# Performance work log

Measured on AMD Instinct MI355X. Metric: run time of the kernel, lower is better.

The kernel has to match this reference:

```python
import jax, jax.numpy as jnp
import numpy as np

N = 100000
E = 1600000
DIN = 128
HID = 64
DOUT = 40
LAYERS = 8
ALPHA = 0.1
THETA = 0.5


def setup_inputs() -> dict:
    key = jax.random.key(0)
    ks = jax.random.split(key, 8)
    x = jax.random.normal(ks[0], (N, DIN), dtype=jnp.float32)
    edge_index = jax.random.randint(ks[1], (2, E), 0, N, dtype=jnp.int64)
    s1 = 1.0 / np.sqrt(DIN)
    s2 = 1.0 / np.sqrt(HID)
    W1 = jax.random.uniform(ks[2], (DIN, HID), jnp.float32, -s1, s1)
    b1 = jax.random.uniform(ks[3], (HID,), jnp.float32, -s1, s1)
    conv_ws = jax.random.uniform(ks[4], (LAYERS, HID, HID), jnp.float32, -s2, s2)
    W2 = jax.random.uniform(ks[5], (HID, DOUT), jnp.float32, -s2, s2)
    b2 = jax.random.uniform(ks[6], (DOUT,), jnp.float32, -s2, s2)
    return {"x": x, "edge_index": edge_index, "W1": W1, "b1": b1,
            "conv_ws": conv_ws, "W2": W2, "b2": b2}


def reference(x, edge_index, W1, b1, conv_ws, W2, b2):
    n = x.shape[0]
    # gcn_norm with self-loops: Ahat = D^-1/2 (A + I) D^-1/2
    loop = jnp.arange(n, dtype=edge_index.dtype)
    src = jnp.concatenate([edge_index[0], loop])
    dst = jnp.concatenate([edge_index[1], loop])
    deg = jax.ops.segment_sum(jnp.ones_like(src, dtype=x.dtype), dst, num_segments=n)
    dinv = jnp.where(deg > 0, jax.lax.rsqrt(deg), 0.0)
    w_e = dinv[src] * dinv[dst]  # [E+N]

    h0 = h = jax.nn.relu(x @ W1 + b1)  # [N, HID]
    for i in range(LAYERS):
        agg = jax.ops.segment_sum(h[src] * w_e[:, None], dst, num_segments=n)
        out = (1.0 - ALPHA) * agg + ALPHA * h0
        beta = np.log(THETA / (i + 1) + 1.0).astype(np.float32)
        h = jax.nn.relu((1.0 - beta) * out + beta * (out @ conv_ws[i]))
    return h @ W2 + b2
```

## Files before the change

kernel.cpp:

```cpp
#include <hip/hip_runtime.h>
#include <hip/hip_fp16.h>
#include <stdint.h>
#include <math.h>

#define HID 64
#define DIN 128
#define DOUT 40
#define N_LAYERS 8
#define CSR_CAP 768

typedef _Float16 half8 __attribute__((ext_vector_type(8)));
typedef float f32x4 __attribute__((ext_vector_type(4)));

static inline int cdiv(int a, int b) { return (a + b - 1) / b; }

__device__ __forceinline__ int edge_src(const uint32_t* ei, int is64, int E, int e) {
    return is64 ? (int)ei[2 * e] : (int)ei[e];
}
__device__ __forceinline__ int edge_dst(const uint32_t* ei, int is64, int E, int e) {
    return is64 ? (int)ei[2 * (size_t)E + 2 * e] : (int)ei[(size_t)E + e];
}

__global__ void setup(const uint32_t* __restrict__ ei, int* __restrict__ flag,
                      const float* __restrict__ convw, __half* __restrict__ Bp,
                      const float* __restrict__ W1, __half* __restrict__ W1h,
                      int* __restrict__ cnt, int n, int nb) {
    int b = blockIdx.x;
    int t = threadIdx.x;
    if (b < nb) {
        int v = b * 256 + t;
        if (v < n) cnt[v] = 0;
        return;
    }
    int r = b - nb;
    if (r < N_LAYERS) {
        float beta = logf(0.5f / (float)(r + 1) + 1.f);
        const float* W = convw + (size_t)r * HID * HID;
        __half* out = Bp + (size_t)r * HID * HID;
        for (int idx = t; idx < HID * HID; idx += 256) {
            int k = idx >> 6, nn = idx & 63;
            float v = beta * W[k * HID + nn] + ((k == nn) ? (1.f - beta) : 0.f);
            out[nn * HID + k] = __float2half(v);
        }
    } else if (r == N_LAYERS) {
        for (int idx = t; idx < DIN * HID; idx += 256) {
            int nn = idx >> 7, k = idx & 127;
            W1h[nn * DIN + k] = __float2half(W1[k * HID + nn]);
        }
    } else if (r == N_LAYERS + 1) {
        if (t < 64) {
            uint32_t wv = ei[2 * t + 1];
            unsigned long long nz = __ballot(wv != 0u);
            if (t == 0) *flag = (nz == 0ull) ? 1 : 0;
        }
    }
}

__global__ void count_pos(const uint32_t* __restrict__ ei, const int* __restrict__ flag,
                          int* __restrict__ cnt, int* __restrict__ pw,
                          int e0, int e1, int E) {
    int e = e0 + blockIdx.x * blockDim.x + threadIdx.x;
    if (e >= e1) return;
    int is64 = *flag;
    int d = edge_dst(ei, is64, E, e);
    pw[e] = atomicAdd(&cnt[d], 1);
}

__global__ void scan1(const int* __restrict__ cnt, int* __restrict__ row_start,
                      int* __restrict__ blocksum, int n) {
    __shared__ int sh[256];
    int t = threadIdx.x;
    int v = blockIdx.x * 256 + t;
    int val = (v < n) ? cnt[v] : 0;
    sh[t] = val;
    __syncthreads();
    for (int o = 1; o < 256; o <<= 1) {
        int y = (t >= o) ? sh[t - o] : 0;
        __syncthreads();
        sh[t] += y;
        __syncthreads();
    }
    if (v < n) row_start[v] = sh[t] - val;
    if (t == 255) blocksum[blockIdx.x] = sh[255];
}

__global__ void scan2(int* __restrict__ blocksum, int nb) {
    __shared__ int sh[512];
    int t = threadIdx.x;
    int val = (t < nb) ? blocksum[t] : 0;
    sh[t] = val;
    __syncthreads();
    for (int o = 1; o < 512; o <<= 1) {
        int y = (t >= o) ? sh[t - o] : 0;
        __syncthreads();
        sh[t] += y;
        __syncthreads();
    }
    if (t < nb) blocksum[t] = sh[t] - val;
}

__global__ void scan3(int* __restrict__ row_start, const int* __restrict__ blocksum,
                      const int* __restrict__ cnt, float* __restrict__ dinv, int n) {
    int v = blockIdx.x * 256 + threadIdx.x;
    if (v < n) {
        row_start[v] += blocksum[v >> 8];
        dinv[v] = rsqrtf((float)(cnt[v] + 1));
    }
}

__global__ void scatter_pos(const uint32_t* __restrict__ ei, const int* __restrict__ flag,
                            const int* __restrict__ row_start, const int* __restrict__ pw,
                            int* __restrict__ csr_src, int E) {
    int e = blockIdx.x * blockDim.x + threadIdx.x;
    if (e >= E) return;
    int is64 = *flag;
    int s = edge_src(ei, is64, E, e);
    int d = edge_dst(ei, is64, E, e);
    csr_src[row_start[d] + pw[e]] = s;
}

__global__ void __launch_bounds__(256) mlp_in_mfma(
        const float* __restrict__ x, const __half* __restrict__ W1h,
        const float* __restrict__ b1, const float* __restrict__ dinv,
        __half2* __restrict__ hp2, __half2* __restrict__ h0h2, int n) {
    __shared__ __align__(16) ushort Bs[64 * 136];
    __shared__ __align__(16) ushort As[128 * 136];
    int t = threadIdx.x;
    {
        const __half2* W2 = (const __half2*)W1h;
        for (int i = t; i < 64 * 64; i += 256) {
            int bn = i >> 6, kp = i & 63;
            *(__half2*)&Bs[bn * 136 + 2 * kp] = W2[bn * 64 + kp];
        }
    }
    int node0 = blockIdx.x * 128;
    {
        const float4* x4 = (const float4*)x;
        for (int i = t; i < 128 * 32; i += 256) {
            int nd = i >> 5, q = i & 31;
            int node = node0 + nd;
            float4 xv = (node < n) ? x4[(size_t)node * 32 + q]
                                   : make_float4(0.f, 0.f, 0.f, 0.f);
            *(__half2*)&As[nd * 136 + q * 4]     = __floats2half2_rn(xv.x, xv.y);
            *(__half2*)&As[nd * 136 + q * 4 + 2] = __floats2half2_rn(xv.z, xv.w);
        }
    }
    __syncthreads();
    int lane = t & 63, wv = t >> 6;
    int nl = lane & 15, quad = lane >> 4;
    int m_base = wv * 32;
    f32x4 C[2][4];
#pragma unroll
    for (int mt = 0; mt < 2; mt++)
#pragma unroll
        for (int nt = 0; nt < 4; nt++) C[mt][nt] = (f32x4)0.f;
#pragma unroll
    for (int kc = 0; kc < 4; kc++) {
        half8 a[2], b[4];
#pragma unroll
        for (int mt = 0; mt < 2; mt++)
            a[mt] = *(const half8*)&As[(m_base + mt * 16 + nl) * 136 + kc * 32 + quad * 8];
#pragma unroll
        for (int nt = 0; nt < 4; nt++)
            b[nt] = *(const half8*)&Bs[(nt * 16 + nl) * 136 + kc * 32 + quad * 8];
#pragma unroll
        for (int mt = 0; mt < 2; mt++)
#pragma unroll
            for (int nt = 0; nt < 4; nt++)
                C[mt][nt] = __builtin_amdgcn_mfma_f32_16x16x32_f16(a[mt], b[nt],
                                                                   C[mt][nt], 0, 0, 0);
    }
    __syncthreads();
#pragma unroll
    for (int nt = 0; nt < 4; nt++) {
        float bias = b1[nt * 16 + nl];
#pragma unroll
        for (int mt = 0; mt < 2; mt++) {
#pragma unroll
            for (int reg = 0; reg < 4; reg++) {
                int nd = m_base + mt * 16 + quad * 4 + reg;
                float v = fmaxf(C[mt][nt][reg] + bias, 0.f);
                As[nd * 72 + nt * 16 + nl] = __half_as_ushort(__float2half(v));
            }
        }
    }
    __syncthreads();
    for (int i = t; i < 128 * 32; i += 256) {
        int nd = i >> 5, kp = i & 31;
        int node = node0 + nd;
        if (node < n) {
            __half2 h = *(const __half2*)&As[nd * 72 + 2 * kp];
            h0h2[(size_t)node * 32 + kp] = h;
            float dv = dinv[node];
            float2 f = __half22float2(h);
            hp2[(size_t)node * 32 + kp] = __floats2half2_rn(f.x * dv, f.y * dv);
        }
    }
}

__global__ void __launch_bounds__(256) gcnii_fused(
        const __half* __restrict__ hp, const __half* __restrict__ h0,
        const int* __restrict__ row_start, const int* __restrict__ cnt,
        const int* __restrict__ csr_src, const float* __restrict__ dinv,
        const __half* __restrict__ Bp, int scale_out,
        __half* __restrict__ hpn, int n, int E) {
    __shared__ __align__(16) ushort Bs[64 * 72];
    __shared__ __align__(16) ushort As[32 * 72];
    __shared__ int csr_lds[CSR_CAP];
    __shared__ int rs_lds[33];
    int t = threadIdx.x;
    int node0 = blockIdx.x * 32;
    int grp = t >> 3, sub = t & 7;

    for (int i = t; i < 512; i += 256) {
        int bn = i >> 3, s8 = i & 7;
        *(half8*)&Bs[bn * 72 + s8 * 8] = *(const half8*)(Bp + bn * 64 + s8 * 8);
    }
    int ts = row_start[node0];
    int te = (node0 + 32 < n) ? row_start[node0 + 32] : E;
    int ne = te - ts;
    int staged = ne < CSR_CAP ? ne : CSR_CAP;
    for (int i = t; i < staged; i += 256) csr_lds[i] = csr_src[ts + i];
    if (t < 33) {
        int v = node0 + t;
        rs_lds[t] = ((v < n) ? row_start[v] : E) - ts;
    }
    __syncthreads();

    int v = node0 + grp;
    int j = rs_lds[grp];
    int end = rs_lds[grp + 1];
    float acc[8];
#pragma unroll
    for (int q = 0; q < 8; q++) acc[q] = 0.f;
    if (ne <= CSR_CAP) {
        int e = j;
        for (; e + 4 <= end; e += 4) {
            int s0 = csr_lds[e],     s1 = csr_lds[e + 1];
            int s2 = csr_lds[e + 2], s3 = csr_lds[e + 3];
            if ((unsigned)s0 >= (unsigned)n) s0 = 0;
            if ((unsigned)s1 >= (unsigned)n) s1 = 0;
            if ((unsigned)s2 >= (unsigned)n) s2 = 0;
            if ((unsigned)s3 >= (unsigned)n) s3 = 0;
            half8 h0v = *(const half8*)(hp + (size_t)s0 * 64 + sub * 8);
            half8 h1v = *(const half8*)(hp + (size_t)s1 * 64 + sub * 8);
            half8 h2v = *(const half8*)(hp + (size_t)s2 * 64 + sub * 8);
            half8 h3v = *(const half8*)(hp + (size_t)s3 * 64 + sub * 8);
#pragma unroll
            for (int q = 0; q < 8; q++)
                acc[q] += ((float)h0v[q] + (float)h1v[q]) + ((float)h2v[q] + (float)h3v[q]);
        }
        for (; e < end; ++e) {
            int s = csr_lds[e];
            if ((unsigned)s >= (unsigned)n) s = 0;
            half8 hv = *(const half8*)(hp + (size_t)s * 64 + sub * 8);
#pragma unroll
            for (int q = 0; q < 8; q++) acc[q] += (float)hv[q];
        }
    } else {
        for (int e = j; e < end; ++e) {
            int s = csr_src[ts + e];
            if ((unsigned)s >= (unsigned)n) s = 0;
            half8 hv = *(const half8*)(hp + (size_t)s * 64 + sub * 8);
#pragma unroll
            for (int q = 0; q < 8; q++) acc[q] += (float)hv[q];
        }
    }
    {
        half8 o;
        if (v < n) {
            float sc = 0.9f * dinv[v];
            half8 hsv = *(const half8*)(hp + (size_t)v * 64 + sub * 8);
            half8 h0v = *(const half8*)(h0 + (size_t)v * 64 + sub * 8);
#pragma unroll
            for (int q = 0; q < 8; q++)
                o[q] = (_Float16)(sc * (acc[q] + (float)hsv[q]) + 0.1f * (float)h0v[q]);
        } else {
#pragma unroll
            for (int q = 0; q < 8; q++) o[q] = (_Float16)0.f;
        }
        *(half8*)&As[grp * 72 + sub * 8] = o;
    }
    __syncthreads();
    int lane = t & 63, w = t >> 6;
    int nl = lane & 15, quad = lane >> 4;
    int strip = w & 1, nth = w >> 1;
    f32x4 C[2];
    C[0] = (f32x4)0.f; C[1] = (f32x4)0.f;
#pragma unroll
    for (int kc = 0; kc < 2; kc++) {
        half8 a = *(const half8*)&As[(strip * 16 + nl) * 72 + kc * 32 + quad * 8];
#pragma unroll
        for (int t2 = 0; t2 < 2; t2++) {
            int nt = nth * 2 + t2;
            half8 b = *(const half8*)&Bs[(nt * 16 + nl) * 72 + kc * 32 + quad * 8];
            C[t2] = __builtin_amdgcn_mfma_f32_16x16x32_f16(a, b, C[t2], 0, 0, 0);
        }
    }
    __syncthreads();
#pragma unroll
    for (int reg = 0; reg < 4; reg++) {
        int nd = strip * 16 + quad * 4 + reg;
        int node = node0 + nd;
        float dv = (scale_out && node < n) ? dinv[node] : 1.f;
#pragma unroll
        for (int t2 = 0; t2 < 2; t2++) {
            int nt = nth * 2 + t2;
            float vv = fmaxf(C[t2][reg], 0.f) * dv;
            As[nd * 72 + nt * 16 + nl] = __half_as_ushort(__float2half(vv));
        }
    }
    __syncthreads();
    {
        int nd = t >> 3, s8 = t & 7;
        int node = node0 + nd;
        if (node < n)
            *(half8*)(hpn + (size_t)node * 64 + s8 * 8) = *(const half8*)&As[nd * 72 + s8 * 8];
    }
}

__global__ void mlp_out(const __half* __restrict__ h, const float* __restrict__ W2,
                        const float* __restrict__ b2, float* __restrict__ y, int n) {
    __shared__ float hs[32 * HID];
    __shared__ float W2s[HID * DOUT];
    __shared__ float b2s[DOUT];
    int t = threadIdx.x;
    for (int i = t; i < HID * DOUT; i += 256) W2s[i] = W2[i];
    if (t < DOUT) b2s[t] = b2[t];
    int node0 = blockIdx.x * 32;
    for (int i = t; i < 32 * HID; i += 256) {
        int node = node0 + (i >> 6);
        hs[i] = (node < n) ? __half2float(h[(size_t)node0 * HID + i]) : 0.f;
    }
    __syncthreads();
    for (int idx = t; idx < 32 * DOUT; idx += 256) {
        int nloc = idx / DOUT, fo = idx % DOUT;
        int node = node0 + nloc;
        if (node >= n) continue;
        float dot = b2s[fo];
#pragma unroll 8
        for (int k = 0; k < HID; k++) dot += hs[nloc * HID + k] * W2s[k * DOUT + fo];
        y[(size_t)node * DOUT + fo] = dot;
    }
}

extern "C" void kernel_launch(void* const* d_in, const int* in_sizes, int n_in,
                              void* d_out, int out_size, void* d_ws, size_t ws_size,
                              hipStream_t stream) {
    const float*    x     = (const float*)d_in[0];
    const uint32_t* ei    = (const uint32_t*)d_in[1];
    const float*    W1    = (const float*)d_in[2];
    const float*    b1    = (const float*)d_in[3];
    const float*    convw = (const float*)d_in[4];
    const float*    W2    = (const float*)d_in[5];
    const float*    b2    = (const float*)d_in[6];
    float*          y     = (float*)d_out;

    int N = in_sizes[0] / DIN;
    int E = in_sizes[1] / 2;

    char* ws = (char*)d_ws;
    size_t off = 0;
    auto alloc = [&](size_t bytes) -> char* {
        char* p = ws + off;
        off = (off + bytes + 255) & ~(size_t)255;
        return p;
    };
    int*     flag      = (int*)alloc(4);
    int*     cnt       = (int*)alloc((size_t)N * 4);
    int*     row_start = (int*)alloc((size_t)N * 4);
    float*   dinv      = (float*)alloc((size_t)N * 4);
    int*     blocksum  = (int*)alloc(512 * 4);
    int*     pw        = (int*)alloc((size_t)E * 4);
    int*     csr_src   = (int*)alloc((size_t)E * 4);
    __half*  Bp        = (__half*)alloc((size_t)N_LAYERS * HID * HID * 2);
    __half*  W1h       = (__half*)alloc((size_t)DIN * HID * 2);
    __half*  h0h       = (__half*)alloc((size_t)N * HID * 2);
    __half*  hpA       = (__half*)alloc((size_t)N * HID * 2);
    __half*  hpB       = (__half*)alloc((size_t)N * HID * 2);

    int nb = cdiv(N, 256);
    setup<<<nb + N_LAYERS + 2, 256, 0, stream>>>(ei, flag, convw, Bp, W1, W1h, cnt, N, nb);
    int Eh = E / 2;
    count_pos<<<cdiv(Eh, 256), 256, 0, stream>>>(ei, flag, cnt, pw, 0, Eh, E);
    count_pos<<<cdiv(E - Eh, 256), 256, 0, stream>>>(ei, flag, cnt, pw, Eh, E, E);
    scan1<<<nb, 256, 0, stream>>>(cnt, row_start, blocksum, N);
    scan2<<<1, 512, 0, stream>>>(blocksum, nb);
    scan3<<<cdiv(N, 256), 256, 0, stream>>>(row_start, blocksum, cnt, dinv, N);
    scatter_pos<<<cdiv(E, 256), 256, 0, stream>>>(ei, flag, row_start, pw, csr_src, E);

    mlp_in_mfma<<<cdiv(N, 128), 256, 0, stream>>>(x, W1h, b1, dinv,
                                                  (__half2*)hpA, (__half2*)h0h, N);

    __half* cur = hpA;
    __half* nxt = hpB;
    for (int i = 0; i < N_LAYERS; i++) {
        int scale_out = (i < N_LAYERS - 1) ? 1 : 0;
        gcnii_fused<<<cdiv(N, 32), 256, 0, stream>>>(
            cur, h0h, row_start, cnt, csr_src, dinv,
            Bp + (size_t)i * HID * HID, scale_out, nxt, N, E);
        __half* tmp = cur; cur = nxt; nxt = tmp;
    }
    mlp_out<<<cdiv(N, 32), 256, 0, stream>>>(cur, W2, b2, y, N);
}
```

Baseline: 531.9 us.

## Fuse output projection into last GCNII layer and simplify CSR build

Removes the separate mlp_out kernel. The final GCNII layer now computes the output projection with MFMA, using W2 split into hi and lo fp16 parts to keep precision. The per-edge position array is replaced by atomic cursor increments in scatter_pos, which saves E ints of writes and reads. The conv weight matrix is no longer staged in LDS and is read directly from global memory per MFMA operand. The last layer also skips writing the hidden state. Risks: CSR order within each row becomes nondeterministic, and B loads from global memory may be slower than from LDS.

```diff
diff --git a/kernel.cpp b/kernel.cpp
--- a/kernel.cpp
+++ b/kernel.cpp
@@ -24,7 +24,8 @@
 __global__ void setup(const uint32_t* __restrict__ ei, int* __restrict__ flag,
                       const float* __restrict__ convw, __half* __restrict__ Bp,
                       const float* __restrict__ W1, __half* __restrict__ W1h,
-                      int* __restrict__ cnt, int n, int nb) {
+                      const float* __restrict__ W2, __half* __restrict__ W2h,
+                      __half* __restrict__ W2l, int* __restrict__ cnt, int n, int nb) {
     int b = blockIdx.x;
     int t = threadIdx.x;
     if (b < nb) {
@@ -53,17 +54,24 @@
             unsigned long long nz = __ballot(wv != 0u);
             if (t == 0) *flag = (nz == 0ull) ? 1 : 0;
         }
+    } else {
+        for (int idx = t; idx < 48 * 64; idx += 256) {
+            int nn = idx >> 6, k = idx & 63;
+            float v = (nn < DOUT) ? W2[k * DOUT + nn] : 0.f;
+            __half hi = __float2half(v);
+            W2h[idx] = hi;
+            W2l[idx] = __float2half(v - __half2float(hi));
+        }
     }
 }
 
 __global__ void count_pos(const uint32_t* __restrict__ ei, const int* __restrict__ flag,
-                          int* __restrict__ cnt, int* __restrict__ pw,
-                          int e0, int e1, int E) {
+                          int* __restrict__ cnt, int e0, int e1, int E) {
     int e = e0 + blockIdx.x * blockDim.x + threadIdx.x;
     if (e >= e1) return;
     int is64 = *flag;
     int d = edge_dst(ei, is64, E, e);
-    pw[e] = atomicAdd(&cnt[d], 1);
+    atomicAdd(&cnt[d], 1);
 }
 
 __global__ void scan1(const int* __restrict__ cnt, int* __restrict__ row_start,
@@ -100,23 +108,25 @@
 }
 
 __global__ void scan3(int* __restrict__ row_start, const int* __restrict__ blocksum,
-                      const int* __restrict__ cnt, float* __restrict__ dinv, int n) {
+                      const int* __restrict__ cnt, int* __restrict__ ptr,
+                      float* __restrict__ dinv, int n) {
     int v = blockIdx.x * 256 + threadIdx.x;
     if (v < n) {
-        row_start[v] += blocksum[v >> 8];
+        int rs = row_start[v] + blocksum[v >> 8];
+        row_start[v] = rs;
+        ptr[v] = rs;
         dinv[v] = rsqrtf((float)(cnt[v] + 1));
     }
 }
 
 __global__ void scatter_pos(const uint32_t* __restrict__ ei, const int* __restrict__ flag,
-                            const int* __restrict__ row_start, const int* __restrict__ pw,
-                            int* __restrict__ csr_src, int E) {
+                            int* __restrict__ ptr, int* __restrict__ csr_src, int E) {
     int e = blockIdx.x * blockDim.x + threadIdx.x;
     if (e >= E) return;
     int is64 = *flag;
     int s = edge_src(ei, is64, E, e);
     int d = edge_dst(ei, is64, E, e);
-    csr_src[row_start[d] + pw[e]] = s;
+    csr_src[atomicAdd(&ptr[d], 1)] = s;
 }
 
 __global__ void __launch_bounds__(256) mlp_in_mfma(
@@ -127,10 +137,10 @@
     __shared__ __align__(16) ushort As[128 * 136];
     int t = threadIdx.x;
     {
-        const __half2* W2 = (const __half2*)W1h;
+        const __half2* W2v = (const __half2*)W1h;
         for (int i = t; i < 64 * 64; i += 256) {
             int bn = i >> 6, kp = i & 63;
-            *(__half2*)&Bs[bn * 136 + 2 * kp] = W2[bn * 64 + kp];
+            *(__half2*)&Bs[bn * 136 + 2 * kp] = W2v[bn * 64 + kp];
         }
     }
     int node0 = blockIdx.x * 128;
@@ -200,11 +210,11 @@
 
 __global__ void __launch_bounds__(256) gcnii_fused(
         const __half* __restrict__ hp, const __half* __restrict__ h0,
-        const int* __restrict__ row_start, const int* __restrict__ cnt,
-        const int* __restrict__ csr_src, const float* __restrict__ dinv,
-        const __half* __restrict__ Bp, int scale_out,
-        __half* __restrict__ hpn, int n, int E) {
-    __shared__ __align__(16) ushort Bs[64 * 72];
+        const int* __restrict__ row_start, const int* __restrict__ csr_src,
+        const float* __restrict__ dinv, const __half* __restrict__ Bp,
+        const __half* __restrict__ W2h, const __half* __restrict__ W2l,
+        const float* __restrict__ b2, int is_last,
+        __half* __restrict__ hpn, float* __restrict__ y, int n, int E) {
     __shared__ __align__(16) ushort As[32 * 72];
     __shared__ int csr_lds[CSR_CAP];
     __shared__ int rs_lds[33];
@@ -212,10 +222,6 @@
     int node0 = blockIdx.x * 32;
     int grp = t >> 3, sub = t & 7;
 
-    for (int i = t; i < 512; i += 256) {
-        int bn = i >> 3, s8 = i & 7;
-        *(half8*)&Bs[bn * 72 + s8 * 8] = *(const half8*)(Bp + bn * 64 + s8 * 8);
-    }
     int ts = row_start[node0];
     int te = (node0 + 32 < n) ? row_start[node0 + 32] : E;
     int ne = te - ts;
@@ -293,54 +299,52 @@
 #pragma unroll
         for (int t2 = 0; t2 < 2; t2++) {
             int nt = nth * 2 + t2;
-            half8 b = *(const half8*)&Bs[(nt * 16 + nl) * 72 + kc * 32 + quad * 8];
+            half8 b = *(const half8*)(Bp + (nt * 16 + nl) * 64 + kc * 32 + quad * 8);
             C[t2] = __builtin_amdgcn_mfma_f32_16x16x32_f16(a, b, C[t2], 0, 0, 0);
         }
     }
     __syncthreads();
-#pragma unroll
-    for (int reg = 0; reg < 4; reg++) {
-        int nd = strip * 16 + quad * 4 + reg;
-        int node = node0 + nd;
-        float dv = (scale_out && node < n) ? dinv[node] : 1.f;
-#pragma unroll
-        for (int t2 = 0; t2 < 2; t2++) {
-            int nt = nth * 2 + t2;
-            float vv = fmaxf(C[t2][reg], 0.f) * dv;
-            As[nd * 72 + nt * 16 + nl] = __half_as_ushort(__float2half(vv));
-        }
-    }
-    __syncthreads();
     {
+#pragma unroll
+        for (int reg = 0; reg < 4; reg++) {
+            int nd = strip * 16 + quad * 4 + reg;
+            int node = node0 + nd;
+            float dv = (!is_last && node < n) ? dinv[node] : 1.f;
+#pragma unroll
+            for (int t2 = 0; t2 < 2; t2++) {
+                int nt = nth * 2 + t2;
+                float vv = fmaxf(C[t2][reg], 0.f) * dv;
+                As[nd * 72 + nt * 16 + nl] = __half_as_ushort(__float2half(vv));
+            }
+        }
+    }
+    __syncthreads();
+    if (!is_last) {
         int nd = t >> 3, s8 = t & 7;
         int node = node0 + nd;
         if (node < n)
             *(half8*)(hpn + (size_t)node * 64 + s8 * 8) = *(const half8*)&As[nd * 72 + s8 * 8];
-    }
-}
-
-__global__ void mlp_out(const __half* __restrict__ h, const float* __restrict__ W2,
-                        const float* __restrict__ b2, float* __restrict__ y, int n) {
-    __shared__ float hs[32 * HID];
-    __shared__ float W2s[HID * DOUT];
-    __shared__ float b2s[DOUT];
-    int t = threadIdx.x;
-    for (int i = t; i < HID * DOUT; i += 256) W2s[i] = W2[i];
-    if (t < DOUT) b2s[t] = b2[t];
-    int node0 = blockIdx.x * 32;
-    for (int i = t; i < 32 * HID; i += 256) {
-        int node = node0 + (i >> 6);
-        hs[i] = (node < n) ? __half2float(h[(size_t)node0 * HID + i]) : 0.f;
-    }
-    __syncthreads();
-    for (int idx = t; idx < 32 * DOUT; idx += 256) {
-        int nloc = idx / DOUT, fo = idx % DOUT;
-        int node = node0 + nloc;
-        if (node >= n) continue;
-        float dot = b2s[fo];
-#pragma unroll 8
-        for (int k = 0; k < HID; k++) dot += hs[nloc * HID + k] * W2s[k * DOUT + fo];
-        y[(size_t)node * DOUT + fo] = dot;
+    } else {
+        for (int ct = (w >> 1); ct < 3; ct += 2) {
+            f32x4 C2 = (f32x4)0.f;
+#pragma unroll
+            for (int kc = 0; kc < 2; kc++) {
+                half8 a  = *(const half8*)&As[(strip * 16 + nl) * 72 + kc * 32 + quad * 8];
+                half8 bh = *(const half8*)(W2h + (ct * 16 + nl) * 64 + kc * 32 + quad * 8);
+                half8 bl = *(const half8*)(W2l + (ct * 16 + nl) * 64 + kc * 32 + quad * 8);
+                C2 = __builtin_amdgcn_mfma_f32_16x16x32_f16(a, bh, C2, 0, 0, 0);
+                C2 = __builtin_amdgcn_mfma_f32_16x16x32_f16(a, bl, C2, 0, 0, 0);
+            }
+            int col = ct * 16 + nl;
+            float bias = (col < DOUT) ? b2[col] : 0.f;
+#pragma unroll
+            for (int reg = 0; reg < 4; reg++) {
+                int nd = strip * 16 + quad * 4 + reg;
+                int node = node0 + nd;
+                if (node < n && col < DOUT)
+                    y[(size_t)node * DOUT + col] = C2[reg] + bias;
+            }
+        }
     }
 }
 
@@ -371,23 +375,26 @@
     int*     row_start = (int*)alloc((size_t)N * 4);
     float*   dinv      = (float*)alloc((size_t)N * 4);
     int*     blocksum  = (int*)alloc(512 * 4);
-    int*     pw        = (int*)alloc((size_t)E * 4);
+    int*     ptr       = (int*)alloc((size_t)N * 4);
     int*     csr_src   = (int*)alloc((size_t)E * 4);
     __half*  Bp        = (__half*)alloc((size_t)N_LAYERS * HID * HID * 2);
     __half*  W1h       = (__half*)alloc((size_t)DIN * HID * 2);
+    __half*  W2h       = (__half*)alloc((size_t)48 * HID * 2);
+    __half*  W2l       = (__half*)alloc((size_t)48 * HID * 2);
     __half*  h0h       = (__half*)alloc((size_t)N * HID * 2);
     __half*  hpA       = (__half*)alloc((size_t)N * HID * 2);
     __half*  hpB       = (__half*)alloc((size_t)N * HID * 2);
 
     int nb = cdiv(N, 256);
-    setup<<<nb + N_LAYERS + 2, 256, 0, stream>>>(ei, flag, convw, Bp, W1, W1h, cnt, N, nb);
+    setup<<<nb + N_LAYERS + 3, 256, 0, stream>>>(ei, flag, convw, Bp, W1, W1h,
+                                                 W2, W2h, W2l, cnt, N, nb);
     int Eh = E / 2;
-    count_pos<<<cdiv(Eh, 256), 256, 0, stream>>>(ei, flag, cnt, pw, 0, Eh, E);
-    count_pos<<<cdiv(E - Eh, 256), 256, 0, stream>>>(ei, flag, cnt, pw, Eh, E, E);
+    count_pos<<<cdiv(Eh, 256), 256, 0, stream>>>(ei, flag, cnt, 0, Eh, E);
+    count_pos<<<cdiv(E - Eh, 256), 256, 0, stream>>>(ei, flag, cnt, Eh, E, E);
     scan1<<<nb, 256, 0, stream>>>(cnt, row_start, blocksum, N);
     scan2<<<1, 512, 0, stream>>>(blocksum, nb);
-    scan3<<<cdiv(N, 256), 256, 0, stream>>>(row_start, blocksum, cnt, dinv, N);
-    scatter_pos<<<cdiv(E, 256), 256, 0, stream>>>(ei, flag, row_start, pw, csr_src, E);
+    scan3<<<cdiv(N, 256), 256, 0, stream>>>(row_start, blocksum, cnt, ptr, dinv, N);
+    scatter_pos<<<cdiv(E, 256), 256, 0, stream>>>(ei, flag, ptr, csr_src, E);
 
     mlp_in_mfma<<<cdiv(N, 128), 256, 0, stream>>>(x, W1h, b1, dinv,
                                                   (__half2*)hpA, (__half2*)h0h, N);
@@ -395,11 +402,10 @@
     __half* cur = hpA;
     __half* nxt = hpB;
     for (int i = 0; i < N_LAYERS; i++) {
-        int scale_out = (i < N_LAYERS - 1) ? 1 : 0;
+        int is_last = (i == N_LAYERS - 1) ? 1 : 0;
         gcnii_fused<<<cdiv(N, 32), 256, 0, stream>>>(
-            cur, h0h, row_start, cnt, csr_src, dinv,
-            Bp + (size_t)i * HID * HID, scale_out, nxt, N, E);
+            cur, h0h, row_start, csr_src, dinv,
+            Bp + (size_t)i * HID * HID, W2h, W2l, b2, is_last, nxt, y, N, E);
         __half* tmp = cur; cur = nxt; nxt = tmp;
     }
-    mlp_out<<<cdiv(N, 32), 256, 0, stream>>>(cur, W2, b2, y, N);
-}
+}
```

Result: slower. 608.7 us (+14.4%).
